# Kernel optimization log

Hardware: AMD Instinct MI355X
Metric: run time of the kernel (lower is better)

The kernel has to match this reference:

```python
import jax, jax.numpy as jnp
import numpy as np
import math

SCALES = (128.0, 256.0, 512.0)
RATIOS = (0.5, 1.0, 2.0)
NMS_THR = 0.7
PRENMS_TOPK = 6000
POSTNMS_TOPK = 300
LOG_MAX = math.log(1000.0 / 16)  # clamp on dw/dh, as in torch code


def conv2d(x, w, b, pad):
    y = jax.lax.conv_general_dilated(x, w, (1, 1), [(pad, pad), (pad, pad)],
                                     dimension_numbers=('NCHW', 'OIHW', 'NCHW'))
    return y + b[None, :, None, None]


def generate_anchors(img_h, img_w, feat_h, feat_w):
    stride_h = img_h // feat_h
    stride_w = img_w // feat_w
    base = []
    for s in SCALES:
        for r in RATIOS:
            w = s * math.sqrt(1.0 / r)
            h = s * math.sqrt(r)
            base.append([-w / 2, -h / 2, w / 2, h / 2])
    base = jnp.asarray(base, jnp.float32)  # [A,4]
    sx = jnp.arange(feat_w, dtype=jnp.float32) * stride_w + stride_w // 2
    sy = jnp.arange(feat_h, dtype=jnp.float32) * stride_h + stride_h // 2
    syy, sxx = jnp.meshgrid(sy, sx, indexing='ij')
    sxf = sxx.reshape(-1)
    syf = syy.reshape(-1)
    shifts = jnp.stack([sxf, syf, sxf, syf], axis=1)  # [HW,4]
    anchors = (shifts[:, None, :] + base[None, :, :]).reshape(-1, 4)  # [HW*A,4]
    return anchors


def decode(reg, anchors):
    # reg, anchors: [N,4]
    w = anchors[:, 2] - anchors[:, 0]
    h = anchors[:, 3] - anchors[:, 1]
    cx = anchors[:, 0] + 0.5 * w
    cy = anchors[:, 1] + 0.5 * h
    dx, dy = reg[:, 0], reg[:, 1]
    dw = jnp.minimum(reg[:, 2], LOG_MAX)
    dh = jnp.minimum(reg[:, 3], LOG_MAX)
    pcx = dx * w + cx
    pcy = dy * h + cy
    pw = jnp.exp(dw) * w
    ph = jnp.exp(dh) * h
    return jnp.stack([pcx - 0.5 * pw, pcy - 0.5 * ph,
                      pcx + 0.5 * pw, pcy + 0.5 * ph], axis=1)


def nms_fixed(boxes, scores, thr, k):
    # Greedy NMS, fixed k iterations; suppressed/invalid entries have score -inf.
    x1, y1, x2, y2 = boxes[:, 0], boxes[:, 1], boxes[:, 2], boxes[:, 3]
    areas = (x2 - x1) * (y2 - y1)

    def step(live, _):
        best = jnp.argmax(live)
        ok = live[best] > -jnp.inf
        b = boxes[best]
        xl = jnp.maximum(b[0], x1)
        yt = jnp.maximum(b[1], y1)
        xr = jnp.minimum(b[2], x2)
        yb = jnp.minimum(b[3], y2)
        inter = jnp.clip(xr - xl, 0.0) * jnp.clip(yb - yt, 0.0)
        iou = inter / (areas[best] + areas - inter)
        live = jnp.where(iou > thr, -jnp.inf, live).at[best].set(-jnp.inf)
        return live, (best.astype(jnp.int32), ok)

    _, (keep, valid) = jax.lax.scan(step, scores, None, length=k)
    return keep, valid


def setup_inputs() -> dict:
    key = jax.random.key(0)
    ks = jax.random.split(key, 6)
    C = 512
    A = len(SCALES) * len(RATIOS)
    return {
        'image': jax.random.normal(ks[0], (8, 3, 1024, 1024), jnp.float32),
        'feat': jax.random.normal(ks[1], (8, C, 64, 64), jnp.float32),
        'conv_w': jax.random.normal(ks[2], (C, C, 3, 3), jnp.float32) * 0.01,
        'conv_b': jnp.zeros((C,), jnp.float32),
        'cls_w': jax.random.normal(ks[3], (A, C, 1, 1), jnp.float32) * 0.01,
        'cls_b': jnp.zeros((A,), jnp.float32),
        'reg_w': jax.random.normal(ks[4], (4 * A, C, 1, 1), jnp.float32) * 0.01,
        'reg_b': jnp.zeros((4 * A,), jnp.float32),
    }


def reference(image, feat, conv_w, conv_b, cls_w, cls_b, reg_w, reg_b):
    t = jax.nn.relu(conv2d(feat, conv_w, conv_b, 1))
    cls = conv2d(t, cls_w, cls_b, 0)   # [B,A,H,W]
    reg = conv2d(t, reg_w, reg_b, 0)   # [B,4A,H,W]
    B, _, H, W = cls.shape
    img_h, img_w = image.shape[-2], image.shape[-1]
    anchors = generate_anchors(img_h, img_w, H, W)  # [H*W*A,4]

    cls0 = cls[0].transpose(1, 2, 0).reshape(-1)        # permute(0,2,3,1): H,W,A order
    reg0 = reg[0].transpose(1, 2, 0).reshape(-1, 4)
    proposals = decode(reg0, anchors)
    scores = jax.nn.sigmoid(jax.lax.stop_gradient(cls0))  # cls_scores.detach()

    k = min(PRENMS_TOPK, scores.shape[0])
    top_scores, top_idx = jax.lax.top_k(scores, k)
    props = proposals[top_idx]
    props = jnp.stack([jnp.clip(props[:, 0], 0.0, float(img_w)),
                       jnp.clip(props[:, 1], 0.0, float(img_h)),
                       jnp.clip(props[:, 2], 0.0, float(img_w)),
                       jnp.clip(props[:, 3], 0.0, float(img_h))], axis=1)
    wv = props[:, 2] - props[:, 0]
    hv = props[:, 3] - props[:, 1]
    valid = (wv >= 1.0) & (hv >= 1.0)   # tiny boxes masked out instead of filtered
    sc = jnp.where(valid, top_scores, -jnp.inf)

    keep, kvalid = nms_fixed(jax.lax.stop_gradient(props), sc, NMS_THR, POSTNMS_TOPK)
    out_boxes = jnp.where(kvalid[:, None], props[keep], 0.0)   # [300,4]
    out_scores = jnp.where(kvalid, top_scores[keep], 0.0)      # [300]
    return jnp.concatenate([out_boxes, out_scores[:, None]], axis=1)  # [300,5]
```

## Files before the change

kernel.cpp:

```cpp
#include <hip/hip_runtime.h>
#include <math.h>

#define NMS_THRESH 0.7f
#define NANCH 36864
#define TOPK 6000
#define NWORDS 94
#define POSTK 300
#define MAXCAND 10240

__global__ __launch_bounds__(256, 2)
void k_conv(const float* __restrict__ feat, const float* __restrict__ W,
            const float* __restrict__ bias, float* __restrict__ tout)
{
    __shared__ float sF[2 * 6528];
    __shared__ float sW[16 * 10 * 16];

    const int blk = blockIdx.x;
    const int ct  = blk & 31;
    const int yt  = blk >> 5;
    const int cob = ct << 4;
    const int y0  = yt << 2;
    const int tid = threadIdx.x;
    const int lane = tid & 63;
    const int wid = __builtin_amdgcn_readfirstlane(tid >> 6);
    const int co0 = cob + (wid << 2);
    const int cwo = wid << 2;
    const int ly = lane >> 4;
    const int lx = (lane & 15) << 2;

    int g_ofs[7]; int l_ofs[7]; bool g_ok[7]; bool w_do[7];
    #pragma unroll
    for (int q = 0; q < 7; ++q) {
        int u = q * 256 + tid;
        int ci = u / 102; int rem = u - ci * 102;
        int rr = rem / 17; int seg = rem - rr * 17;
        int gy = y0 - 1 + rr;
        w_do[q] = (u < 1632);
        g_ok[q] = w_do[q] && (seg < 16) && (gy >= 0) && (gy < 64);
        g_ofs[q] = ((ci & 15) << 12) + ((gy & 63) << 6) + ((seg & 15) << 2);
        l_ofs[q] = ci * 408 + rr * 68 + (seg << 2);
    }

    const int sci = tid >> 4, sco = tid & 15;
    const float* wsrc = W + (size_t)(cob + sco) * 4608 + sci * 9;

    float acc[4][4];
    #pragma unroll
    for (int i = 0; i < 4; ++i)
        #pragma unroll
        for (int j = 0; j < 4; ++j) acc[i][j] = 0.f;

    float wreg[9];
    {
        float4 r0[7];
        #pragma unroll
        for (int q = 0; q < 7; ++q)
            r0[q] = g_ok[q] ? *(const float4*)(feat + g_ofs[q])
                            : make_float4(0.f, 0.f, 0.f, 0.f);
        #pragma unroll
        for (int q = 0; q < 7; ++q)
            if (w_do[q]) *(float4*)&sF[l_ofs[q]] = r0[q];
        #pragma unroll
        for (int t = 0; t < 9; ++t) wreg[t] = wsrc[t];
    }

    int p = 0;
    for (int cc = 0; cc < 32; ++cc) {
        const bool more = cc < 31;
        #pragma unroll
        for (int t = 0; t < 9; ++t)
            sW[sci * 160 + t * 16 + sco] = wreg[t];
        float4 r[7]; float wregN[9];
        if (more) {
            const float* fsrc = feat + ((size_t)(cc + 1) << 16);
            #pragma unroll
            for (int q = 0; q < 7; ++q)
                r[q] = g_ok[q] ? *(const float4*)(fsrc + g_ofs[q])
                               : make_float4(0.f, 0.f, 0.f, 0.f);
            const float* wp = wsrc + (size_t)(cc + 1) * 144;
            #pragma unroll
            for (int t = 0; t < 9; ++t) wregN[t] = wp[t];
        }
        __syncthreads();
        const int pbase = p * 6528;
        #pragma unroll 2
        for (int ci = 0; ci < 16; ++ci) {
            #pragma unroll
            for (int ky = 0; ky < 3; ++ky) {
                const float* rb = sF + pbase + ci * 408 + (ly + ky) * 68;
                float4 f4 = *(const float4*)&rb[lx];
                int c0 = lx ? lx - 1 : 0;
                int c5 = (lx < 60) ? lx + 4 : 63;
                float t0 = rb[c0];
                float t5 = rb[c5];
                float fr[6];
                fr[0] = lx ? t0 : 0.f;
                fr[1] = f4.x; fr[2] = f4.y; fr[3] = f4.z; fr[4] = f4.w;
                fr[5] = (lx < 60) ? t5 : 0.f;
                const float* wb = sW + ci * 160 + (ky * 3) * 16 + cwo;
                float w_[3][4];
                *(float4*)w_[0] = *(const float4*)(wb);
                *(float4*)w_[1] = *(const float4*)(wb + 16);
                *(float4*)w_[2] = *(const float4*)(wb + 32);
                #pragma unroll
                for (int kx = 0; kx < 3; ++kx)
                    #pragma unroll
                    for (int i = 0; i < 4; ++i)
                        #pragma unroll
                        for (int j = 0; j < 4; ++j)
                            acc[i][j] = fmaf(fr[i + kx], w_[kx][j], acc[i][j]);
            }
        }
        if (more) {
            const int wb2 = (p ^ 1) * 6528;
            #pragma unroll
            for (int q = 0; q < 7; ++q)
                if (w_do[q]) *(float4*)&sF[wb2 + l_ofs[q]] = r[q];
            #pragma unroll
            for (int t = 0; t < 9; ++t) wreg[t] = wregN[t];
        }
        __syncthreads();
        p ^= 1;
    }

    const int y = y0 + ly;
    #pragma unroll
    for (int j = 0; j < 4; ++j) {
        const float bv = bias[co0 + j];
        float4 o;
        o.x = fmaxf(acc[0][j] + bv, 0.f);
        o.y = fmaxf(acc[1][j] + bv, 0.f);
        o.z = fmaxf(acc[2][j] + bv, 0.f);
        o.w = fmaxf(acc[3][j] + bv, 0.f);
        *(float4*)&tout[((size_t)(co0 + j) << 12) + (y << 6) + lx] = o;
    }
}

__global__ __launch_bounds__(64)
void k_heads(const float* __restrict__ t, const float* __restrict__ cls_w,
             const float* __restrict__ cls_b, const float* __restrict__ reg_w,
             const float* __restrict__ reg_b, float* __restrict__ heads)
{
    const int bid = blockIdx.x;
    const int ch = bid % 45;
    const int pt = bid / 45;
    const int px = (pt << 6) + threadIdx.x;
    const float* wp; float bv;
    if (ch < 9) { wp = cls_w + ch * 512;       bv = cls_b[ch]; }
    else        { wp = reg_w + (ch - 9) * 512; bv = reg_b[ch - 9]; }
    float acc = bv;
    #pragma unroll 8
    for (int ci = 0; ci < 512; ++ci)
        acc = fmaf(t[((size_t)ci << 12) + px], wp[ci], acc);
    heads[((size_t)ch << 12) + px] = acc;
}

__global__ void k_decode(const float* __restrict__ heads,
                         float* __restrict__ score, float* __restrict__ validf,
                         float* __restrict__ box, unsigned* __restrict__ hist)
{
    __shared__ unsigned lh[4096];
    const int tid = threadIdx.x;
    for (int q = tid; q < 4096; q += 256) lh[q] = 0u;
    __syncthreads();

    int idx = blockIdx.x * 256 + tid;
    int p = idx / 9, a = idx - p * 9;
    int yq = p >> 6, xq = p & 63;
    const double scl[3] = {128.0, 256.0, 512.0};
    const double rat[3] = {0.5, 1.0, 2.0};
    double s = scl[a / 3], r = rat[a % 3];
    float bw = (float)(s * sqrt(1.0 / r) * 0.5);
    float bh = (float)(s * sqrt(r) * 0.5);
    float sx = xq * 16.0f + 8.0f;
    float sy = yq * 16.0f + 8.0f;
    float a0 = sx - bw, a1 = sy - bh, a2 = sx + bw, a3 = sy + bh;
    float wa = a2 - a0, ha = a3 - a1;
    float cx = a0 + 0.5f * wa, cy = a1 + 0.5f * ha;
    float logit = heads[(size_t)a * 4096 + p];
    float dx = heads[(size_t)(9  + 4 * a) * 4096 + p];
    float dy = heads[(size_t)(10 + 4 * a) * 4096 + p];
    float dw = fminf(heads[(size_t)(11 + 4 * a) * 4096 + p], 4.135166556742356f);
    float dh = fminf(heads[(size_t)(12 + 4 * a) * 4096 + p], 4.135166556742356f);
    float pcx = dx * wa + cx, pcy = dy * ha + cy;
    float pw = expf(dw) * wa, ph = expf(dh) * ha;
    float x1 = pcx - 0.5f * pw, y1 = pcy - 0.5f * ph;
    float x2 = pcx + 0.5f * pw, y2 = pcy + 0.5f * ph;
    x1 = fminf(fmaxf(x1, 0.f), 1024.f); y1 = fminf(fmaxf(y1, 0.f), 1024.f);
    x2 = fminf(fmaxf(x2, 0.f), 1024.f); y2 = fminf(fmaxf(y2, 0.f), 1024.f);
    float wv = x2 - x1, hv = y2 - y1;
    float sc = 1.f / (1.f + expf(-logit));
    score[idx]  = sc;
    validf[idx] = (wv >= 1.f && hv >= 1.f) ? 1.f : 0.f;
    box[idx * 4 + 0] = x1; box[idx * 4 + 1] = y1;
    box[idx * 4 + 2] = x2; box[idx * 4 + 3] = y2;

    atomicAdd(&lh[__float_as_uint(sc) >> 19], 1u);
    __syncthreads();
    for (int q = tid; q < 4096; q += 256) if (lh[q]) atomicAdd(&hist[q], lh[q]);
}

__global__ void k_zero(unsigned* __restrict__ p) {
    int i = blockIdx.x * 256 + threadIdx.x;
    if (i < 8448) p[i] = 0u;
}

__global__ void k_cut1(const unsigned* __restrict__ hist, unsigned* __restrict__ meta) {
    __shared__ unsigned hh[4096];
    __shared__ unsigned gs[256];
    int tid = threadIdx.x;
    for (int q = tid; q < 4096; q += 256) hh[q] = hist[q];
    __syncthreads();
    unsigned s = 0;
    #pragma unroll
    for (int k = 0; k < 16; ++k) s += hh[tid * 16 + k];
    gs[tid] = s;
    __syncthreads();
    if (tid == 0) {
        unsigned cum = 0;
        for (int g = 255; g >= 0; --g) {
            if (cum + gs[g] >= (unsigned)TOPK) {
                for (int b = g * 16 + 15; b >= g * 16; --b) {
                    if (cum + hh[b] >= (unsigned)TOPK) { meta[2] = (unsigned)b; meta[3] = cum; break; }
                    cum += hh[b];
                }
                break;
            }
            cum += gs[g];
        }
    }
}

__global__ void k_hist2(const float* __restrict__ score, const unsigned* __restrict__ meta,
                        unsigned* __restrict__ hist2) {
    int idx = blockIdx.x * 256 + threadIdx.x;
    unsigned bits = __float_as_uint(score[idx]);
    if ((bits >> 19) == meta[2]) atomicAdd(&hist2[(bits >> 7) & 0xFFFu], 1u);
}

__global__ void k_cut2(const unsigned* __restrict__ hist2, unsigned* __restrict__ meta) {
    __shared__ unsigned hh[4096];
    __shared__ unsigned gs[256];
    int tid = threadIdx.x;
    for (int q = tid; q < 4096; q += 256) hh[q] = hist2[q];
    __syncthreads();
    unsigned s = 0;
    #pragma unroll
    for (int k = 0; k < 16; ++k) s += hh[tid * 16 + k];
    gs[tid] = s;
    __syncthreads();
    if (tid == 0) {
        unsigned cum = meta[3];
        unsigned B = meta[2];
        unsigned cut = B << 19;
        for (int g = 255; g >= 0; --g) {
            if (cum + gs[g] >= (unsigned)TOPK) {
                for (int b = g * 16 + 15; b >= g * 16; --b) {
                    cum += hh[b];
                    if (cum >= (unsigned)TOPK) { cut = (B << 19) | ((unsigned)b << 7); break; }
                }
                break;
            }
            cum += gs[g];
        }
        meta[0] = cut;
    }
}

__global__ void k_compact(const float* __restrict__ score, unsigned* __restrict__ meta,
                          int* __restrict__ cand, float* __restrict__ cscore) {
    int idx = blockIdx.x * 256 + threadIdx.x;
    unsigned bits = __float_as_uint(score[idx]);
    if (bits >= meta[0]) {
        unsigned pos = atomicAdd(&meta[1], 1u);
        if (pos < (unsigned)MAXCAND) {
            cand[pos] = idx;
            cscore[pos] = __uint_as_float(bits);
        }
    }
}

__global__ __launch_bounds__(256, 4)
void k_rank(const float* __restrict__ score, const float* __restrict__ validf,
            const float* __restrict__ box, const unsigned* __restrict__ meta,
            const int* __restrict__ cand, const float* __restrict__ cscore,
            float* __restrict__ score6, float* __restrict__ sc6,
            float* __restrict__ box6)
{
    __shared__ int pc[8][32];
    const int tid = threadIdx.x;
    const int il = tid & 31, js = tid >> 5;
    unsigned ncand = meta[1]; if (ncand > (unsigned)MAXCAND) ncand = MAXCAND;
    const int c = blockIdx.x * 32 + il;
    int i = -1; float si = 0.f;
    if (c < (int)ncand) { i = cand[c]; si = cscore[c]; }
    int cnt = 0;
    {
        const float4* cs4 = (const float4*)cscore;
        const int4*   cd4 = (const int4*)cand;
        const int q0 = js * 320;
        for (int q = 0; q < 320; ++q) {
            float4 v = cs4[q0 + q];
            int4   w = cd4[q0 + q];
            cnt += (v.x > si) || (v.x == si && w.x < i);
            cnt += (v.y > si) || (v.y == si && w.y < i);
            cnt += (v.z > si) || (v.z == si && w.z < i);
            cnt += (v.w > si) || (v.w == si && w.w < i);
        }
    }
    pc[js][il] = cnt;
    __syncthreads();
    if (js == 0 && i >= 0) {
        int rank = 0;
        #pragma unroll
        for (int q = 0; q < 8; ++q) rank += pc[q][il];
        if (rank < TOPK) {
            score6[rank] = si;
            sc6[rank] = (validf[i] != 0.f) ? si : -INFINITY;
            box6[rank * 4 + 0] = box[i * 4 + 0];
            box6[rank * 4 + 1] = box[i * 4 + 1];
            box6[rank * 4 + 2] = box[i * 4 + 2];
            box6[rank * 4 + 3] = box[i * 4 + 3];
        }
    }
}

__global__ __launch_bounds__(512)
void k_nms(const float* __restrict__ sc6, const float* __restrict__ score6,
           const float* __restrict__ box6, float* __restrict__ out)
{
    __shared__ float kx1[POSTK], ky1[POSTK], kx2[POSTK], ky2[POSTK], kar[POSTK];
    __shared__ int kidx[POSTK];
    __shared__ unsigned long long pOR[8];
    __shared__ int kcnt_s;
    const int tid = threadIdx.x, lane = tid & 63, wv = tid >> 6;

    if (tid == 0) kcnt_s = 0;
    int i0 = lane;
    float cx1 = box6[i0 * 4 + 0], cy1 = box6[i0 * 4 + 1];
    float cx2 = box6[i0 * 4 + 2], cy2 = box6[i0 * 4 + 3];
    float csc = sc6[i0];
    __syncthreads();

    for (int b = 0; b < NWORDS; ++b) {
        float nx1 = 0.f, ny1 = 0.f, nx2 = 0.f, ny2 = 0.f, nsc = -INFINITY;
        if (b + 1 < NWORDS) {
            int ni = (b + 1) * 64 + lane; if (ni >= TOPK) ni = TOPK - 1;
            nx1 = box6[ni * 4 + 0]; ny1 = box6[ni * 4 + 1];
            nx2 = box6[ni * 4 + 2]; ny2 = box6[ni * 4 + 3];
            nsc = sc6[ni];
        }
        const int i = b * 64 + lane;
        const bool v = (i < TOPK) && (csc > -INFINITY);
        const float ar = (cx2 - cx1) * (cy2 - cy1);
        const int kc = kcnt_s;
        bool dead = false;
        for (int j = wv; j < kc; j += 8) {
            float xl = fmaxf(kx1[j], cx1), yt = fmaxf(ky1[j], cy1);
            float xr = fminf(kx2[j], cx2), yb = fminf(ky2[j], cy2);
            float inter = fmaxf(xr - xl, 0.f) * fmaxf(yb - yt, 0.f);
            float iou = inter / (kar[j] + ar - inter);
            dead = dead || (iou > NMS_THRESH);
        }
        pOR[wv] = __ballot(dead);
        __syncthreads();
        if (wv == 0) {
            unsigned long long supp = pOR[0] | pOR[1] | pOR[2] | pOR[3]
                                    | pOR[4] | pOR[5] | pOR[6] | pOR[7];
            unsigned long long validb = __ballot(v);
            unsigned long long cand2 = validb & ~supp;
            int kc2 = kc;
            while (cand2 != 0ull && kc2 < POSTK) {
                int rr = __builtin_ctzll(cand2);
                float rx1 = __shfl(cx1, rr, 64), ry1 = __shfl(cy1, rr, 64);
                float rx2 = __shfl(cx2, rr, 64), ry2 = __shfl(cy2, rr, 64);
                float rar = __shfl(ar, rr, 64);
                if (lane == 0) {
                    kx1[kc2] = rx1; ky1[kc2] = ry1;
                    kx2[kc2] = rx2; ky2[kc2] = ry2;
                    kar[kc2] = rar; kidx[kc2] = b * 64 + rr;
                }
                float xl = fmaxf(rx1, cx1), yt = fmaxf(ry1, cy1);
                float xr = fminf(rx2, cx2), yb = fminf(ry2, cy2);
                float inter = fmaxf(xr - xl, 0.f) * fmaxf(yb - yt, 0.f);
                float iou = inter / (rar + ar - inter);
                unsigned long long sm = __ballot(iou > NMS_THRESH) | (1ull << rr);
                cand2 &= ~sm;
                ++kc2;
            }
            if (lane == 0) kcnt_s = kc2;
        }
        __syncthreads();
        if (kcnt_s >= POSTK) break;
        cx1 = nx1; cy1 = ny1; cx2 = nx2; cy2 = ny2; csc = nsc;
    }

    const int kc = kcnt_s;
    for (int n = tid; n < POSTK; n += 512) {
        float o0 = 0.f, o1 = 0.f, o2 = 0.f, o3 = 0.f, o4 = 0.f;
        if (n < kc) {
            int i = kidx[n];
            o0 = box6[i * 4 + 0]; o1 = box6[i * 4 + 1];
            o2 = box6[i * 4 + 2]; o3 = box6[i * 4 + 3];
            o4 = score6[i];
        }
        out[n * 5 + 0] = o0; out[n * 5 + 1] = o1; out[n * 5 + 2] = o2;
        out[n * 5 + 3] = o3; out[n * 5 + 4] = o4;
    }
}

extern "C" void kernel_launch(void* const* d_in, const int* in_sizes, int n_in,
                              void* d_out, int out_size, void* d_ws, size_t ws_size,
                              hipStream_t stream)
{
    (void)in_sizes; (void)n_in; (void)out_size; (void)ws_size;
    const float* feat   = (const float*)d_in[1];
    const float* conv_w = (const float*)d_in[2];
    const float* conv_b = (const float*)d_in[3];
    const float* cls_w  = (const float*)d_in[4];
    const float* cls_b  = (const float*)d_in[5];
    const float* reg_w  = (const float*)d_in[6];
    const float* reg_b  = (const float*)d_in[7];

    char* ws = (char*)d_ws;
    float*    t      = (float*)(ws + 0);
    float*    heads  = (float*)(ws + 8388608);
    unsigned* hist   = (unsigned*)(ws + 9125888);
    unsigned* hist2  = (unsigned*)(ws + 9142272);
    unsigned* meta   = (unsigned*)(ws + 9158656);
    int*      cand   = (int*)(ws + 9158720);
    float*    cscore = (float*)(ws + 9199680);
    float*    score  = (float*)(ws + 9240640);
    float*    validf = (float*)(ws + 9388096);
    float*    box    = (float*)(ws + 9535552);
    float*    score6 = (float*)(ws + 10125376);
    float*    sc6    = (float*)(ws + 10149952);
    float*    box6   = (float*)(ws + 10174528);

    k_zero   <<<33,   256, 0, stream>>>(hist);
    k_conv   <<<512,  256, 0, stream>>>(feat, conv_w, conv_b, t);
    k_heads  <<<2880, 64,  0, stream>>>(t, cls_w, cls_b, reg_w, reg_b, heads);
    k_decode <<<144,  256, 0, stream>>>(heads, score, validf, box, hist);
    k_cut1   <<<1,    256, 0, stream>>>(hist, meta);
    k_hist2  <<<144,  256, 0, stream>>>(score, meta, hist2);
    k_cut2   <<<1,    256, 0, stream>>>(hist2, meta);
    k_compact<<<144,  256, 0, stream>>>(score, meta, cand, cscore);
    k_rank   <<<320,  256, 0, stream>>>(score, validf, box, meta, cand, cscore, score6, sc6, box6);
    k_nms    <<<1,    512, 0, stream>>>(sc6, score6, box6, (float*)d_out);
}
```

Before: 520.7 us.

## Give each conv thread eight output channels using two-wave 128-thread blocks

The 3x3 conv kernel now runs 128 threads per block (two waves) instead of 256. Each thread accumulates 4 pixels by 8 output channels rather than 4 by 4, so every feature value read from shared memory feeds twice as many FMAs. Staging loops, weight loading (now paired float2 stores into a padded 172-stride sW) and launch bounds are adjusted to match. The cost is more registers per thread, more load work per thread, and fewer resident waves per CU, which may hurt latency hiding.

```diff
diff --git a/kernel.cpp b/kernel.cpp
--- a/kernel.cpp
+++ b/kernel.cpp
@@ -8,12 +8,12 @@
 #define POSTK 300
 #define MAXCAND 10240
 
-__global__ __launch_bounds__(256, 2)
+__global__ __launch_bounds__(128, 1)
 void k_conv(const float* __restrict__ feat, const float* __restrict__ W,
             const float* __restrict__ bias, float* __restrict__ tout)
 {
     __shared__ float sF[2 * 6528];
-    __shared__ float sW[16 * 10 * 16];
+    __shared__ float sW[16 * 172];
 
     const int blk = blockIdx.x;
     const int ct  = blk & 31;
@@ -23,63 +23,67 @@
     const int tid = threadIdx.x;
     const int lane = tid & 63;
     const int wid = __builtin_amdgcn_readfirstlane(tid >> 6);
-    const int co0 = cob + (wid << 2);
-    const int cwo = wid << 2;
+    const int cwo = wid << 3;
+    const int co0 = cob + cwo;
     const int ly = lane >> 4;
     const int lx = (lane & 15) << 2;
 
-    int g_ofs[7]; int l_ofs[7]; bool g_ok[7]; bool w_do[7];
+    int g_ofs[13]; int l_ofs[13]; bool g_ok[13]; bool w_do[13];
     #pragma unroll
-    for (int q = 0; q < 7; ++q) {
-        int u = q * 256 + tid;
+    for (int q = 0; q < 13; ++q) {
+        int u = q * 128 + tid;
         int ci = u / 102; int rem = u - ci * 102;
         int rr = rem / 17; int seg = rem - rr * 17;
         int gy = y0 - 1 + rr;
         w_do[q] = (u < 1632);
         g_ok[q] = w_do[q] && (seg < 16) && (gy >= 0) && (gy < 64);
         g_ofs[q] = ((ci & 15) << 12) + ((gy & 63) << 6) + ((seg & 15) << 2);
-        l_ofs[q] = ci * 408 + rr * 68 + (seg << 2);
-    }
-
-    const int sci = tid >> 4, sco = tid & 15;
-    const float* wsrc = W + (size_t)(cob + sco) * 4608 + sci * 9;
-
-    float acc[4][4];
+        l_ofs[q] = (ci & 15) * 408 + rr * 68 + (seg << 2);
+    }
+
+    const int sci = tid >> 3, sc2 = tid & 7;
+    const float* wsrc0 = W + (size_t)(cob + 2 * sc2) * 4608 + sci * 9;
+    const float* wsrc1 = wsrc0 + 4608;
+
+    float acc[4][8];
     #pragma unroll
     for (int i = 0; i < 4; ++i)
         #pragma unroll
-        for (int j = 0; j < 4; ++j) acc[i][j] = 0.f;
-
-    float wreg[9];
+        for (int j = 0; j < 8; ++j) acc[i][j] = 0.f;
+
+    float wreg[18];
     {
-        float4 r0[7];
-        #pragma unroll
-        for (int q = 0; q < 7; ++q)
+        float4 r0[13];
+        #pragma unroll
+        for (int q = 0; q < 13; ++q)
             r0[q] = g_ok[q] ? *(const float4*)(feat + g_ofs[q])
                             : make_float4(0.f, 0.f, 0.f, 0.f);
         #pragma unroll
-        for (int q = 0; q < 7; ++q)
+        for (int q = 0; q < 13; ++q)
             if (w_do[q]) *(float4*)&sF[l_ofs[q]] = r0[q];
         #pragma unroll
-        for (int t = 0; t < 9; ++t) wreg[t] = wsrc[t];
+        for (int t = 0; t < 9; ++t) { wreg[t] = wsrc0[t]; wreg[9 + t] = wsrc1[t]; }
     }
 
     int p = 0;
     for (int cc = 0; cc < 32; ++cc) {
         const bool more = cc < 31;
         #pragma unroll
-        for (int t = 0; t < 9; ++t)
-            sW[sci * 160 + t * 16 + sco] = wreg[t];
-        float4 r[7]; float wregN[9];
+        for (int t = 0; t < 9; ++t) {
+            float2 wp2; wp2.x = wreg[t]; wp2.y = wreg[9 + t];
+            *(float2*)&sW[sci * 172 + t * 16 + 2 * sc2] = wp2;
+        }
+        float4 r[13]; float wregN[18];
         if (more) {
             const float* fsrc = feat + ((size_t)(cc + 1) << 16);
             #pragma unroll
-            for (int q = 0; q < 7; ++q)
+            for (int q = 0; q < 13; ++q)
                 r[q] = g_ok[q] ? *(const float4*)(fsrc + g_ofs[q])
                                : make_float4(0.f, 0.f, 0.f, 0.f);
-            const float* wp = wsrc + (size_t)(cc + 1) * 144;
+            const float* wp0 = wsrc0 + (size_t)(cc + 1) * 144;
+            const float* wp1 = wsrc1 + (size_t)(cc + 1) * 144;
             #pragma unroll
-            for (int t = 0; t < 9; ++t) wregN[t] = wp[t];
+            for (int t = 0; t < 9; ++t) { wregN[t] = wp0[t]; wregN[9 + t] = wp1[t]; }
         }
         __syncthreads();
         const int pbase = p * 6528;
@@ -97,27 +101,30 @@
                 fr[0] = lx ? t0 : 0.f;
                 fr[1] = f4.x; fr[2] = f4.y; fr[3] = f4.z; fr[4] = f4.w;
                 fr[5] = (lx < 60) ? t5 : 0.f;
-                const float* wb = sW + ci * 160 + (ky * 3) * 16 + cwo;
-                float w_[3][4];
-                *(float4*)w_[0] = *(const float4*)(wb);
-                *(float4*)w_[1] = *(const float4*)(wb + 16);
-                *(float4*)w_[2] = *(const float4*)(wb + 32);
+                const float* wb = sW + ci * 172 + ky * 48 + cwo;
+                float w_[3][8];
+                *(float4*)&w_[0][0] = *(const float4*)(wb);
+                *(float4*)&w_[0][4] = *(const float4*)(wb + 4);
+                *(float4*)&w_[1][0] = *(const float4*)(wb + 16);
+                *(float4*)&w_[1][4] = *(const float4*)(wb + 20);
+                *(float4*)&w_[2][0] = *(const float4*)(wb + 32);
+                *(float4*)&w_[2][4] = *(const float4*)(wb + 36);
                 #pragma unroll
                 for (int kx = 0; kx < 3; ++kx)
                     #pragma unroll
                     for (int i = 0; i < 4; ++i)
                         #pragma unroll
-                        for (int j = 0; j < 4; ++j)
+                        for (int j = 0; j < 8; ++j)
                             acc[i][j] = fmaf(fr[i + kx], w_[kx][j], acc[i][j]);
             }
         }
         if (more) {
             const int wb2 = (p ^ 1) * 6528;
             #pragma unroll
-            for (int q = 0; q < 7; ++q)
+            for (int q = 0; q < 13; ++q)
                 if (w_do[q]) *(float4*)&sF[wb2 + l_ofs[q]] = r[q];
             #pragma unroll
-            for (int t = 0; t < 9; ++t) wreg[t] = wregN[t];
+            for (int t = 0; t < 18; ++t) wreg[t] = wregN[t];
         }
         __syncthreads();
         p ^= 1;
@@ -125,7 +132,7 @@
 
     const int y = y0 + ly;
     #pragma unroll
-    for (int j = 0; j < 4; ++j) {
+    for (int j = 0; j < 8; ++j) {
         const float bv = bias[co0 + j];
         float4 o;
         o.x = fmaxf(acc[0][j] + bv, 0.f);
@@ -438,7 +445,7 @@
     float*    box6   = (float*)(ws + 10174528);
 
     k_zero   <<<33,   256, 0, stream>>>(hist);
-    k_conv   <<<512,  256, 0, stream>>>(feat, conv_w, conv_b, t);
+    k_conv   <<<512,  128, 0, stream>>>(feat, conv_w, conv_b, t);
     k_heads  <<<2880, 64,  0, stream>>>(t, cls_w, cls_b, reg_w, reg_b, heads);
     k_decode <<<144,  256, 0, stream>>>(heads, score, validf, box, hist);
     k_cut1   <<<1,    256, 0, stream>>>(hist, meta);
```

Measured after the change: 511.3 us. No clear change (-1.8%).
